# Kernel tuning notes

Hardware: AMD Instinct MI355X
Metric: run time of the kernel (lower is better)

The kernel has to match this reference:

```python
import jax, jax.numpy as jnp
import numpy as np

N_NODES = 100000
N_EDGES = 600000
H_DIM = 128


def _gcn_layer(h, src, dst, norm, W, b):
    # m = (h @ W) * norm  -> scatter-sum over edges -> * norm + b -> LeakyReLU(0.2)
    m = jnp.matmul(h, W) * norm                      # [N, H]
    agg = jax.ops.segment_sum(m[src], dst, num_segments=N_NODES)  # [N, H]
    n = agg * norm + b
    return jnp.where(n > 0, n, 0.2 * n)


def setup_inputs() -> dict:
    key = jax.random.key(0)
    ks = jax.random.split(key, 8)
    node_id = jax.random.randint(ks[0], (N_NODES,), 0, N_NODES)
    src = jax.random.randint(ks[1], (N_EDGES,), 0, N_NODES)
    dst = jax.random.randint(ks[2], (N_EDGES,), 0, N_NODES)
    norm = jax.random.uniform(ks[3], (N_NODES, 1), dtype=jnp.float32)
    embed = jax.random.normal(ks[4], (N_NODES, H_DIM), dtype=jnp.float32) * 0.02
    embed = embed.at[0].set(0.0)  # padding_idx=0
    gain = np.sqrt(2.0)  # calculate_gain('relu')
    lim = gain * np.sqrt(6.0 / (H_DIM + H_DIM))
    W1 = jax.random.uniform(ks[5], (H_DIM, H_DIM), jnp.float32, -lim, lim)
    W2 = jax.random.uniform(ks[6], (H_DIM, H_DIM), jnp.float32, -lim, lim)
    stdv = 1.0 / np.sqrt(H_DIM)
    kb1, kb2 = jax.random.split(ks[7])
    b1 = jax.random.uniform(kb1, (H_DIM,), jnp.float32, -stdv, stdv)
    b2 = jax.random.uniform(kb2, (H_DIM,), jnp.float32, -stdv, stdv)
    return {"node_id": node_id, "src": src, "dst": dst, "norm": norm,
            "embed": embed, "W1": W1, "b1": b1, "W2": W2, "b2": b2}


def reference(node_id, src, dst, norm, embed, W1, b1, W2, b2):
    h = embed[node_id]                               # EmbeddingLayer
    h = _gcn_layer(h, src, dst, norm, W1, b1)        # GCNLayer 1
    h = _gcn_layer(h, src, dst, norm, W2, b2)        # GCNLayer 2
    return h
```

## Files before the change

kernel.cpp:

```cpp
#include <hip/hip_runtime.h>

namespace {
constexpr int NN = 100000;
constexpr int NE = 600000;
constexpr int H  = 128;
constexpr int SCAN_B = 256;
constexpr int NBLK_SCAN = (NN + SCAN_B - 1) / SCAN_B;

__global__ __launch_bounds__(256) void write_marker(float* __restrict__ out,
                                                    int n, float val) {
  int i = blockIdx.x * 256 + threadIdx.x;
  if (i < n) out[i] = val;
}


__global__ __launch_bounds__(256) void zero_f4(float4* __restrict__ p, int n4) {
  int i = blockIdx.x * 256 + threadIdx.x;
  if (i < n4) p[i] = float4{0.f, 0.f, 0.f, 0.f};
}

__global__ __launch_bounds__(256) void scatter_l1(
    const int* __restrict__ src, const int* __restrict__ dst,
    const int* __restrict__ node_id, const float* __restrict__ embed,
    const float* __restrict__ norm, float* __restrict__ agg) {
  int idx = blockIdx.x * 256 + threadIdx.x;
  int e = idx >> 5;
  if (e >= NE) return;
  int c = (idx & 31) << 2;
  int s = src[e];
  float nrm = norm[s];
  const float4 v = *reinterpret_cast<const float4*>(embed + (size_t)node_id[s] * H + c);
  float* o = agg + (size_t)dst[e] * H + c;
  atomicAdd(o + 0, v.x * nrm);
  atomicAdd(o + 1, v.y * nrm);
  atomicAdd(o + 2, v.z * nrm);
  atomicAdd(o + 3, v.w * nrm);
}

__global__ __launch_bounds__(256) void scatter_l2(
    const int* __restrict__ src, const int* __restrict__ dst,
    const float* __restrict__ h1, const float* __restrict__ norm,
    float* __restrict__ agg) {
  int idx = blockIdx.x * 256 + threadIdx.x;
  int e = idx >> 5;
  if (e >= NE) return;
  int c = (idx & 31) << 2;
  int s = src[e];
  float nrm = norm[s];
  const float4 v = *reinterpret_cast<const float4*>(h1 + (size_t)s * H + c);
  float* o = agg + (size_t)dst[e] * H + c;
  atomicAdd(o + 0, v.x * nrm);
  atomicAdd(o + 1, v.y * nrm);
  atomicAdd(o + 2, v.z * nrm);
  atomicAdd(o + 3, v.w * nrm);
}

__global__ __launch_bounds__(128) void row_gemm_act(
    const float* __restrict__ agg, const float* __restrict__ W,
    const float* __restrict__ norm, const float* __restrict__ bias,
    float* __restrict__ out) {
  __shared__ float hs[H];
  const int row = blockIdx.x, j = threadIdx.x;
  hs[j] = agg[(size_t)row * H + j];
  __syncthreads();
  float acc = 0.f;
#pragma unroll
  for (int k = 0; k < H; ++k) acc += hs[k] * W[k * H + j];
  float v = acc * norm[row] + bias[j];
  v = v > 0.f ? v : 0.2f * v;
  out[(size_t)row * H + j] = v;
}


__global__ __launch_bounds__(256) void zero_int(int* __restrict__ p, int n) {
  int i = blockIdx.x * 256 + threadIdx.x;
  if (i < n) p[i] = 0;
}

__global__ __launch_bounds__(256) void hist_dst(const int* __restrict__ dst,
                                                int* __restrict__ deg) {
  int e = blockIdx.x * 256 + threadIdx.x;
  if (e < NE) atomicAdd(&deg[dst[e]], 1);
}

__global__ __launch_bounds__(SCAN_B) void scan1(const int* __restrict__ deg,
                                                int* __restrict__ offs,
                                                int* __restrict__ bsums) {
  __shared__ int sh[SCAN_B];
  const int t = threadIdx.x;
  const int gid = blockIdx.x * SCAN_B + t;
  int v = (gid < NN) ? deg[gid] : 0;
  sh[t] = v;
  __syncthreads();
  for (int d = 1; d < SCAN_B; d <<= 1) {
    int add = (t >= d) ? sh[t - d] : 0;
    __syncthreads();
    sh[t] += add;
    __syncthreads();
  }
  if (gid < NN) offs[gid] = sh[t] - v;
  if (t == SCAN_B - 1) bsums[blockIdx.x] = sh[t];
}

__global__ __launch_bounds__(512) void scan2(int* __restrict__ bsums) {
  __shared__ int sh[512];
  const int t = threadIdx.x;
  int v = (t < NBLK_SCAN) ? bsums[t] : 0;
  sh[t] = v;
  __syncthreads();
  for (int d = 1; d < 512; d <<= 1) {
    int add = (t >= d) ? sh[t - d] : 0;
    __syncthreads();
    sh[t] += add;
    __syncthreads();
  }
  if (t < NBLK_SCAN) bsums[t] = sh[t] - v;
}

__global__ __launch_bounds__(256) void scan3(int* __restrict__ offs,
                                             const int* __restrict__ bsums) {
  int gid = blockIdx.x * 256 + threadIdx.x;
  if (gid < NN) offs[gid] += bsums[blockIdx.x];
  if (gid == 0) offs[NN] = NE;
}

__global__ __launch_bounds__(256) void fill_csr(
    const int* __restrict__ src, const int* __restrict__ dst,
    const int* __restrict__ offs, int* __restrict__ cnt, int* __restrict__ csr) {
  int e = blockIdx.x * 256 + threadIdx.x;
  if (e >= NE) return;
  int d = dst[e];
  int pos = offs[d] + atomicAdd(&cnt[d], 1);
  csr[pos] = src[e];
}

template <bool L1>
__global__ __launch_bounds__(256) void gather_rows(
    const int* __restrict__ offs, const int* __restrict__ csr,
    const int* __restrict__ node_id, const float* __restrict__ h,
    const float* __restrict__ norm, float* __restrict__ agg) {
  const int node = blockIdx.x * 8 + (threadIdx.x >> 5);
  const int c = (threadIdx.x & 31) << 2;
  const int beg = offs[node];
  const int end = offs[node + 1];
  float4 acc{0.f, 0.f, 0.f, 0.f};
  for (int i = beg; i < end; ++i) {
    int s = csr[i];
    float nrm = norm[s];
    int row = L1 ? node_id[s] : s;
    const float4 v = *reinterpret_cast<const float4*>(h + (size_t)row * H + c);
    acc.x += v.x * nrm;
    acc.y += v.y * nrm;
    acc.z += v.z * nrm;
    acc.w += v.w * nrm;
  }
  *reinterpret_cast<float4*>(agg + (size_t)node * H + c) = acc;
}

__global__ __launch_bounds__(256) void gemm32_act(
    const float* __restrict__ agg, const float* __restrict__ W,
    const float* __restrict__ norm, const float* __restrict__ bias,
    float* __restrict__ out) {
  __shared__ float Wld[H * H];
  __shared__ float hs[32][H];
  const int t = threadIdx.x;
  const int rowBase = blockIdx.x * 32;

  const float4* W4 = reinterpret_cast<const float4*>(W);
  float4* Wld4 = reinterpret_cast<float4*>(Wld);
#pragma unroll
  for (int i = 0; i < 16; ++i) Wld4[t + i * 256] = W4[t + i * 256];

  {
    const float4* a4 = reinterpret_cast<const float4*>(agg + (size_t)rowBase * H);
    float4* hs4 = reinterpret_cast<float4*>(&hs[0][0]);
#pragma unroll
    for (int i = 0; i < 4; ++i) hs4[t + i * 256] = a4[t + i * 256];
  }
  __syncthreads();

  const int j4 = t & 31;
  const int r0 = t >> 5;
  float4 acc0{0.f, 0.f, 0.f, 0.f}, acc1{0.f, 0.f, 0.f, 0.f};
  float4 acc2{0.f, 0.f, 0.f, 0.f}, acc3{0.f, 0.f, 0.f, 0.f};
#pragma unroll 16
  for (int k = 0; k < H; ++k) {
    const float4 w = Wld4[k * 32 + j4];
    const float a0 = hs[r0][k];
    const float a1 = hs[r0 + 8][k];
    const float a2 = hs[r0 + 16][k];
    const float a3 = hs[r0 + 24][k];
    acc0.x += a0 * w.x; acc0.y += a0 * w.y; acc0.z += a0 * w.z; acc0.w += a0 * w.w;
    acc1.x += a1 * w.x; acc1.y += a1 * w.y; acc1.z += a1 * w.z; acc1.w += a1 * w.w;
    acc2.x += a2 * w.x; acc2.y += a2 * w.y; acc2.z += a2 * w.z; acc2.w += a2 * w.w;
    acc3.x += a3 * w.x; acc3.y += a3 * w.y; acc3.z += a3 * w.z; acc3.w += a3 * w.w;
  }

  const float4 bv = reinterpret_cast<const float4*>(bias)[j4];
#define EMIT(RR, ACC)                                                     \
  {                                                                       \
    const int row = rowBase + (RR);                                       \
    const float nrm = norm[row];                                          \
    float4 o;                                                             \
    o.x = ACC.x * nrm + bv.x; o.x = o.x > 0.f ? o.x : 0.2f * o.x;         \
    o.y = ACC.y * nrm + bv.y; o.y = o.y > 0.f ? o.y : 0.2f * o.y;         \
    o.z = ACC.z * nrm + bv.z; o.z = o.z > 0.f ? o.z : 0.2f * o.z;         \
    o.w = ACC.w * nrm + bv.w; o.w = o.w > 0.f ? o.w : 0.2f * o.w;         \
    *reinterpret_cast<float4*>(out + (size_t)row * H + j4 * 4) = o;       \
  }
  EMIT(r0, acc0)
  EMIT(r0 + 8, acc1)
  EMIT(r0 + 16, acc2)
  EMIT(r0 + 24, acc3)
#undef EMIT
}

}

extern "C" void kernel_launch(void* const* d_in, const int* in_sizes, int n_in,
                              void* d_out, int out_size, void* d_ws, size_t ws_size,
                              hipStream_t stream) {
  float* out = (float*)d_out;
  const int nElem = NN * H;
  const int mkBl  = (out_size + 255) / 256;

  bool order_ok =
      (n_in == 9 && in_sizes[0] == NN && in_sizes[1] == NE && in_sizes[2] == NE &&
       in_sizes[3] == NN && in_sizes[4] == NN * H && in_sizes[5] == H * H &&
       in_sizes[6] == H && in_sizes[7] == H * H && in_sizes[8] == H);
  if (!order_ok || out_size != nElem) {
    write_marker<<<mkBl, 256, 0, stream>>>(out, out_size,
                                           (out_size != nElem) ? 300.0f : 200.0f);
    return;
  }
  if (ws_size < (size_t)nElem * 4) {
    write_marker<<<mkBl, 256, 0, stream>>>(out, out_size,
                                           2.0f + (float)(ws_size >> 20));
    return;
  }

  const int* node_id = (const int*)d_in[0];
  const int* src     = (const int*)d_in[1];
  const int* dst     = (const int*)d_in[2];
  const float* norm  = (const float*)d_in[3];
  const float* embed = (const float*)d_in[4];
  const float* W1    = (const float*)d_in[5];
  const float* b1    = (const float*)d_in[6];
  const float* W2    = (const float*)d_in[7];
  const float* b2    = (const float*)d_in[8];

  float* agg = (float*)d_ws;
  float* h1  = out;

  int* offs  = (int*)((char*)d_ws + (size_t)nElem * 4);
  int* cnt   = offs + (NN + 1);
  int* csr   = cnt + NN;
  int* bsums = csr + NE;
  const size_t need =
      (size_t)nElem * 4 + ((size_t)(NN + 1) + NN + NE + 512) * 4;

  const int zeroNBl = (NN + 255) / 256;
  const int edgeBl  = (NE + 255) / 256;

  if (ws_size >= need) {
    zero_int<<<zeroNBl, 256, 0, stream>>>(cnt, NN);
    hist_dst<<<edgeBl, 256, 0, stream>>>(dst, cnt);
    scan1<<<NBLK_SCAN, SCAN_B, 0, stream>>>(cnt, offs, bsums);
    scan2<<<1, 512, 0, stream>>>(bsums);
    scan3<<<NBLK_SCAN, 256, 0, stream>>>(offs, bsums);
    zero_int<<<zeroNBl, 256, 0, stream>>>(cnt, NN);
    fill_csr<<<edgeBl, 256, 0, stream>>>(src, dst, offs, cnt, csr);

    gather_rows<true><<<NN / 8, 256, 0, stream>>>(offs, csr, node_id, embed, norm, agg);
    gemm32_act<<<NN / 32, 256, 0, stream>>>(agg, W1, norm, b1, h1);

    gather_rows<false><<<NN / 8, 256, 0, stream>>>(offs, csr, node_id, h1, norm, agg);
    gemm32_act<<<NN / 32, 256, 0, stream>>>(agg, W2, norm, b2, out);
    return;
  }

  const int zeroBl = (nElem / 4 + 255) / 256;
  const int scatBl = (NE * 32 + 255) / 256;

  zero_f4<<<zeroBl, 256, 0, stream>>>((float4*)agg, nElem / 4);
  scatter_l1<<<scatBl, 256, 0, stream>>>(src, dst, node_id, embed, norm, agg);
  row_gemm_act<<<NN, 128, 0, stream>>>(agg, W1, norm, b1, h1);

  zero_f4<<<zeroBl, 256, 0, stream>>>((float4*)agg, nElem / 4);
  scatter_l2<<<scatBl, 256, 0, stream>>>(src, dst, h1, norm, agg);
  row_gemm_act<<<NN, 128, 0, stream>>>(agg, W2, norm, b2, out);
}
```

Measured before the change: 396.8 us.

## Pre-gather edge records, fold norm into layer-1 output, enlarge GEMM tile

During CSR build, each edge now stores a packed record of node_id[src] and norm[src]. The layer-1 gather reads that record directly, removing two dependent indirect loads per edge. Layer 1's epilogue pre-multiplies its output by norm, so the layer-2 gather becomes a plain sum over rows. The GEMM moves from 32-row tiles to 128-row tiles with a swizzled shared-memory layout and 8x8 register blocking per thread. Scan3 also seeds the fill cursors, which removes a zero pass. The cost is extra workspace for the records, and the larger tiles use much more LDS and registers, leaving only one block resident per CU.

```diff
diff --git a/kernel.cpp b/kernel.cpp
--- a/kernel.cpp
+++ b/kernel.cpp
@@ -118,24 +118,85 @@
 }
 
 __global__ __launch_bounds__(256) void scan3(int* __restrict__ offs,
-                                             const int* __restrict__ bsums) {
+                                             const int* __restrict__ bsums,
+                                             int* __restrict__ cnt) {
   int gid = blockIdx.x * 256 + threadIdx.x;
-  if (gid < NN) offs[gid] += bsums[blockIdx.x];
+  if (gid < NN) {
+    int v = offs[gid] + bsums[blockIdx.x];
+    offs[gid] = v;
+    cnt[gid] = v;
+  }
   if (gid == 0) offs[NN] = NE;
 }
 
+template <bool WITH_REC>
 __global__ __launch_bounds__(256) void fill_csr(
     const int* __restrict__ src, const int* __restrict__ dst,
-    const int* __restrict__ offs, int* __restrict__ cnt, int* __restrict__ csr) {
+    const int* __restrict__ node_id, const float* __restrict__ norm,
+    int* __restrict__ cnt, int* __restrict__ csr2, int2* __restrict__ rec1) {
   int e = blockIdx.x * 256 + threadIdx.x;
   if (e >= NE) return;
   int d = dst[e];
-  int pos = offs[d] + atomicAdd(&cnt[d], 1);
-  csr[pos] = src[e];
-}
-
-template <bool L1>
-__global__ __launch_bounds__(256) void gather_rows(
+  int s = src[e];
+  int pos = atomicAdd(&cnt[d], 1);
+  csr2[pos] = s;
+  if (WITH_REC) rec1[pos] = make_int2(node_id[s], __float_as_int(norm[s]));
+}
+
+
+__global__ __launch_bounds__(256) void gather_rec(
+    const int* __restrict__ offs, const int2* __restrict__ rec,
+    const float* __restrict__ h, float* __restrict__ agg) {
+  const int node = blockIdx.x * 8 + (threadIdx.x >> 5);
+  const int c = (threadIdx.x & 31) << 2;
+  const int beg = offs[node];
+  const int end = offs[node + 1];
+  float4 acc{0.f, 0.f, 0.f, 0.f}, acc2{0.f, 0.f, 0.f, 0.f};
+  int i = beg;
+  for (; i + 2 <= end; i += 2) {
+    int2 ra = rec[i], rb = rec[i + 1];
+    const float4 va = *reinterpret_cast<const float4*>(h + (size_t)ra.x * H + c);
+    const float4 vb = *reinterpret_cast<const float4*>(h + (size_t)rb.x * H + c);
+    float na = __int_as_float(ra.y), nb = __int_as_float(rb.y);
+    acc.x += va.x * na;  acc.y += va.y * na;  acc.z += va.z * na;  acc.w += va.w * na;
+    acc2.x += vb.x * nb; acc2.y += vb.y * nb; acc2.z += vb.z * nb; acc2.w += vb.w * nb;
+  }
+  if (i < end) {
+    int2 ra = rec[i];
+    const float4 va = *reinterpret_cast<const float4*>(h + (size_t)ra.x * H + c);
+    float na = __int_as_float(ra.y);
+    acc.x += va.x * na; acc.y += va.y * na; acc.z += va.z * na; acc.w += va.w * na;
+  }
+  acc.x += acc2.x; acc.y += acc2.y; acc.z += acc2.z; acc.w += acc2.w;
+  *reinterpret_cast<float4*>(agg + (size_t)node * H + c) = acc;
+}
+
+__global__ __launch_bounds__(256) void gather_idx(
+    const int* __restrict__ offs, const int* __restrict__ csr,
+    const float* __restrict__ h, float* __restrict__ agg) {
+  const int node = blockIdx.x * 8 + (threadIdx.x >> 5);
+  const int c = (threadIdx.x & 31) << 2;
+  const int beg = offs[node];
+  const int end = offs[node + 1];
+  float4 acc{0.f, 0.f, 0.f, 0.f}, acc2{0.f, 0.f, 0.f, 0.f};
+  int i = beg;
+  for (; i + 2 <= end; i += 2) {
+    int r0 = csr[i], r1 = csr[i + 1];
+    const float4 va = *reinterpret_cast<const float4*>(h + (size_t)r0 * H + c);
+    const float4 vb = *reinterpret_cast<const float4*>(h + (size_t)r1 * H + c);
+    acc.x += va.x;  acc.y += va.y;  acc.z += va.z;  acc.w += va.w;
+    acc2.x += vb.x; acc2.y += vb.y; acc2.z += vb.z; acc2.w += vb.w;
+  }
+  if (i < end) {
+    int r0 = csr[i];
+    const float4 va = *reinterpret_cast<const float4*>(h + (size_t)r0 * H + c);
+    acc.x += va.x; acc.y += va.y; acc.z += va.z; acc.w += va.w;
+  }
+  acc.x += acc2.x; acc.y += acc2.y; acc.z += acc2.z; acc.w += acc2.w;
+  *reinterpret_cast<float4*>(agg + (size_t)node * H + c) = acc;
+}
+
+__global__ __launch_bounds__(256) void gather_mid_l1(
     const int* __restrict__ offs, const int* __restrict__ csr,
     const int* __restrict__ node_id, const float* __restrict__ h,
     const float* __restrict__ norm, float* __restrict__ agg) {
@@ -147,72 +208,100 @@
   for (int i = beg; i < end; ++i) {
     int s = csr[i];
     float nrm = norm[s];
-    int row = L1 ? node_id[s] : s;
-    const float4 v = *reinterpret_cast<const float4*>(h + (size_t)row * H + c);
-    acc.x += v.x * nrm;
-    acc.y += v.y * nrm;
-    acc.z += v.z * nrm;
-    acc.w += v.w * nrm;
+    const float4 v = *reinterpret_cast<const float4*>(h + (size_t)node_id[s] * H + c);
+    acc.x += v.x * nrm; acc.y += v.y * nrm; acc.z += v.z * nrm; acc.w += v.w * nrm;
   }
   *reinterpret_cast<float4*>(agg + (size_t)node * H + c) = acc;
 }
 
-__global__ __launch_bounds__(256) void gemm32_act(
+
+#define FMA4(ACC, S, W) \
+  ACC.x += (S) * (W).x; ACC.y += (S) * (W).y; ACC.z += (S) * (W).z; ACC.w += (S) * (W).w;
+
+template <bool SCALE_OUT>
+__global__ __launch_bounds__(256, 1) void gemm128_act(
     const float* __restrict__ agg, const float* __restrict__ W,
     const float* __restrict__ norm, const float* __restrict__ bias,
     float* __restrict__ out) {
-  __shared__ float Wld[H * H];
-  __shared__ float hs[32][H];
+  __shared__ float4 Wld[128 * 32];
+  __shared__ float4 As[128 * 32];
   const int t = threadIdx.x;
-  const int rowBase = blockIdx.x * 32;
+  const int rowBase = blockIdx.x * 128;
 
   const float4* W4 = reinterpret_cast<const float4*>(W);
-  float4* Wld4 = reinterpret_cast<float4*>(Wld);
-#pragma unroll
-  for (int i = 0; i < 16; ++i) Wld4[t + i * 256] = W4[t + i * 256];
-
-  {
-    const float4* a4 = reinterpret_cast<const float4*>(agg + (size_t)rowBase * H);
-    float4* hs4 = reinterpret_cast<float4*>(&hs[0][0]);
-#pragma unroll
-    for (int i = 0; i < 4; ++i) hs4[t + i * 256] = a4[t + i * 256];
+#pragma unroll
+  for (int i = 0; i < 16; ++i) {
+    int g = t + i * 256;
+    int k = g >> 5, c4 = g & 31;
+    int sc4 = (c4 >> 1) + ((c4 & 1) << 4);
+    Wld[k * 32 + sc4] = W4[g];
+  }
+  const float4* A4 = reinterpret_cast<const float4*>(agg) + (size_t)rowBase * 32;
+#pragma unroll
+  for (int i = 0; i < 16; ++i) {
+    int g = t + i * 256;
+    int r = g >> 5, k4 = g & 31;
+    float4 v = (rowBase + r < NN) ? A4[g] : float4{0.f, 0.f, 0.f, 0.f};
+    As[r * 32 + (k4 ^ (r & 7))] = v;
   }
   __syncthreads();
 
-  const int j4 = t & 31;
-  const int r0 = t >> 5;
-  float4 acc0{0.f, 0.f, 0.f, 0.f}, acc1{0.f, 0.f, 0.f, 0.f};
-  float4 acc2{0.f, 0.f, 0.f, 0.f}, acc3{0.f, 0.f, 0.f, 0.f};
-#pragma unroll 16
-  for (int k = 0; k < H; ++k) {
-    const float4 w = Wld4[k * 32 + j4];
-    const float a0 = hs[r0][k];
-    const float a1 = hs[r0 + 8][k];
-    const float a2 = hs[r0 + 16][k];
-    const float a3 = hs[r0 + 24][k];
-    acc0.x += a0 * w.x; acc0.y += a0 * w.y; acc0.z += a0 * w.z; acc0.w += a0 * w.w;
-    acc1.x += a1 * w.x; acc1.y += a1 * w.y; acc1.z += a1 * w.z; acc1.w += a1 * w.w;
-    acc2.x += a2 * w.x; acc2.y += a2 * w.y; acc2.z += a2 * w.z; acc2.w += a2 * w.w;
-    acc3.x += a3 * w.x; acc3.y += a3 * w.y; acc3.z += a3 * w.z; acc3.w += a3 * w.w;
-  }
-
-  const float4 bv = reinterpret_cast<const float4*>(bias)[j4];
-#define EMIT(RR, ACC)                                                     \
-  {                                                                       \
-    const int row = rowBase + (RR);                                       \
-    const float nrm = norm[row];                                          \
-    float4 o;                                                             \
-    o.x = ACC.x * nrm + bv.x; o.x = o.x > 0.f ? o.x : 0.2f * o.x;         \
-    o.y = ACC.y * nrm + bv.y; o.y = o.y > 0.f ? o.y : 0.2f * o.y;         \
-    o.z = ACC.z * nrm + bv.z; o.z = o.z > 0.f ? o.z : 0.2f * o.z;         \
-    o.w = ACC.w * nrm + bv.w; o.w = o.w > 0.f ? o.w : 0.2f * o.w;         \
-    *reinterpret_cast<float4*>(out + (size_t)row * H + j4 * 4) = o;       \
-  }
-  EMIT(r0, acc0)
-  EMIT(r0 + 8, acc1)
-  EMIT(r0 + 16, acc2)
-  EMIT(r0 + 24, acc3)
-#undef EMIT
+  const int j8 = t & 15;
+  const int r0 = t >> 4;
+  float4 accA[8], accB[8];
+#pragma unroll
+  for (int i = 0; i < 8; ++i) {
+    accA[i] = float4{0.f, 0.f, 0.f, 0.f};
+    accB[i] = float4{0.f, 0.f, 0.f, 0.f};
+  }
+
+#pragma unroll 4
+  for (int k4 = 0; k4 < 32; ++k4) {
+    const int kb = k4 * 128;
+    float4 wa0 = Wld[kb + j8],       wb0 = Wld[kb + j8 + 16];
+    float4 wa1 = Wld[kb + 32 + j8],  wb1 = Wld[kb + 32 + j8 + 16];
+    float4 wa2 = Wld[kb + 64 + j8],  wb2 = Wld[kb + 64 + j8 + 16];
+    float4 wa3 = Wld[kb + 96 + j8],  wb3 = Wld[kb + 96 + j8 + 16];
+#pragma unroll
+    for (int i = 0; i < 8; ++i) {
+      const int row = r0 + 16 * i;
+      float4 a = As[row * 32 + (k4 ^ (row & 7))];
+      FMA4(accA[i], a.x, wa0) FMA4(accB[i], a.x, wb0)
+      FMA4(accA[i], a.y, wa1) FMA4(accB[i], a.y, wb1)
+      FMA4(accA[i], a.z, wa2) FMA4(accB[i], a.z, wb2)
+      FMA4(accA[i], a.w, wa3) FMA4(accB[i], a.w, wb3)
+    }
+  }
+
+  const float4 bv0 = reinterpret_cast<const float4*>(bias)[2 * j8];
+  const float4 bv1 = reinterpret_cast<const float4*>(bias)[2 * j8 + 1];
+#pragma unroll
+  for (int i = 0; i < 8; ++i) {
+    const int row = rowBase + r0 + 16 * i;
+    if (row < NN) {
+      const float nrm = norm[row];
+      float4 o0, o1;
+      o0.x = accA[i].x * nrm + bv0.x; o0.y = accA[i].y * nrm + bv0.y;
+      o0.z = accA[i].z * nrm + bv0.z; o0.w = accA[i].w * nrm + bv0.w;
+      o1.x = accB[i].x * nrm + bv1.x; o1.y = accB[i].y * nrm + bv1.y;
+      o1.z = accB[i].z * nrm + bv1.z; o1.w = accB[i].w * nrm + bv1.w;
+      o0.x = o0.x > 0.f ? o0.x : 0.2f * o0.x;
+      o0.y = o0.y > 0.f ? o0.y : 0.2f * o0.y;
+      o0.z = o0.z > 0.f ? o0.z : 0.2f * o0.z;
+      o0.w = o0.w > 0.f ? o0.w : 0.2f * o0.w;
+      o1.x = o1.x > 0.f ? o1.x : 0.2f * o1.x;
+      o1.y = o1.y > 0.f ? o1.y : 0.2f * o1.y;
+      o1.z = o1.z > 0.f ? o1.z : 0.2f * o1.z;
+      o1.w = o1.w > 0.f ? o1.w : 0.2f * o1.w;
+      if (SCALE_OUT) {
+        o0.x *= nrm; o0.y *= nrm; o0.z *= nrm; o0.w *= nrm;
+        o1.x *= nrm; o1.y *= nrm; o1.z *= nrm; o1.w *= nrm;
+      }
+      float4* op = reinterpret_cast<float4*>(out + (size_t)row * H + j8 * 8);
+      op[0] = o0;
+      op[1] = o1;
+    }
+  }
 }
 
 }
@@ -250,32 +339,48 @@
   const float* b2    = (const float*)d_in[8];
 
   float* agg = (float*)d_ws;
-  float* h1  = out;
-
-  int* offs  = (int*)((char*)d_ws + (size_t)nElem * 4);
+  float* h1n = out;
+  int2* rec1 = (int2*)((char*)d_ws + (size_t)nElem * 4);
+  int* csr2  = (int*)(rec1 + NE);
+  int* offs  = csr2 + NE;
   int* cnt   = offs + (NN + 1);
-  int* csr   = cnt + NN;
-  int* bsums = csr + NE;
-  const size_t need =
-      (size_t)nElem * 4 + ((size_t)(NN + 1) + NN + NE + 512) * 4;
+  int* bsums = cnt + NN;
+
+  const size_t need_mid =
+      (size_t)nElem * 4 + ((size_t)NE + (NN + 1) + NN + 512) * 4;
+  const size_t need_full = need_mid + (size_t)NE * 8;
 
   const int zeroNBl = (NN + 255) / 256;
   const int edgeBl  = (NE + 255) / 256;
-
-  if (ws_size >= need) {
+  const int gemmBl  = (NN + 127) / 128;
+
+  if (ws_size >= need_mid) {
+    const bool full = (ws_size >= need_full);
+    if (!full) {
+      csr2  = (int*)((char*)d_ws + (size_t)nElem * 4);
+      offs  = csr2 + NE;
+      cnt   = offs + (NN + 1);
+      bsums = cnt + NN;
+    }
+
     zero_int<<<zeroNBl, 256, 0, stream>>>(cnt, NN);
     hist_dst<<<edgeBl, 256, 0, stream>>>(dst, cnt);
     scan1<<<NBLK_SCAN, SCAN_B, 0, stream>>>(cnt, offs, bsums);
     scan2<<<1, 512, 0, stream>>>(bsums);
-    scan3<<<NBLK_SCAN, 256, 0, stream>>>(offs, bsums);
-    zero_int<<<zeroNBl, 256, 0, stream>>>(cnt, NN);
-    fill_csr<<<edgeBl, 256, 0, stream>>>(src, dst, offs, cnt, csr);
-
-    gather_rows<true><<<NN / 8, 256, 0, stream>>>(offs, csr, node_id, embed, norm, agg);
-    gemm32_act<<<NN / 32, 256, 0, stream>>>(agg, W1, norm, b1, h1);
-
-    gather_rows<false><<<NN / 8, 256, 0, stream>>>(offs, csr, node_id, h1, norm, agg);
-    gemm32_act<<<NN / 32, 256, 0, stream>>>(agg, W2, norm, b2, out);
+    scan3<<<NBLK_SCAN, 256, 0, stream>>>(offs, bsums, cnt);
+    if (full)
+      fill_csr<true><<<edgeBl, 256, 0, stream>>>(src, dst, node_id, norm, cnt, csr2, rec1);
+    else
+      fill_csr<false><<<edgeBl, 256, 0, stream>>>(src, dst, node_id, norm, cnt, csr2, nullptr);
+
+    if (full)
+      gather_rec<<<NN / 8, 256, 0, stream>>>(offs, rec1, embed, agg);
+    else
+      gather_mid_l1<<<NN / 8, 256, 0, stream>>>(offs, csr2, node_id, embed, norm, agg);
+    gemm128_act<true><<<gemmBl, 256, 0, stream>>>(agg, W1, norm, b1, h1n);
+
+    gather_idx<<<NN / 8, 256, 0, stream>>>(offs, csr2, h1n, agg);
+    gemm128_act<false><<<gemmBl, 256, 0, stream>>>(agg, W2, norm, b2, out);
     return;
   }
 
@@ -284,9 +389,9 @@
 
   zero_f4<<<zeroBl, 256, 0, stream>>>((float4*)agg, nElem / 4);
   scatter_l1<<<scatBl, 256, 0, stream>>>(src, dst, node_id, embed, norm, agg);
-  row_gemm_act<<<NN, 128, 0, stream>>>(agg, W1, norm, b1, h1);
+  row_gemm_act<<<NN, 128, 0, stream>>>(agg, W1, norm, b1, out);
 
   zero_f4<<<zeroBl, 256, 0, stream>>>((float4*)agg, nElem / 4);
-  scatter_l2<<<scatBl, 256, 0, stream>>>(src, dst, h1, norm, agg);
+  scatter_l2<<<scatBl, 256, 0, stream>>>(src, dst, out, norm, agg);
   row_gemm_act<<<NN, 128, 0, stream>>>(agg, W2, norm, b2, out);
 }
```

New measurement: 438.7 us. 10.6% more time.
